# Kernel optimization log

Measured on AMD Instinct MI355X. Metric: run time of the kernel, lower is better.

## Reference

```python
import jax, jax.numpy as jnp
import numpy as np

# cfg.SIAMESE constants (typical FastVOD values)
ROIS_PER_IMAGE = 128
FG_PER_IMAGE = 32          # round(0.25 * 128)
FG_THRESH = 0.7
BG_THRESH_HI = 0.3
BG_THRESH_LO = 0.0

B, N, G = 16, 65536, 64


def _make_boxes(key, shape, img=1000.0):
    k1, k2, k3, k4 = jax.random.split(key, 4)
    x1 = jax.random.uniform(k1, shape) * (img - 64.0)
    y1 = jax.random.uniform(k2, shape) * (img - 64.0)
    w = jax.random.uniform(k3, shape) * 200.0 + 8.0
    h = jax.random.uniform(k4, shape) * 200.0 + 8.0
    return jnp.stack([x1, y1, jnp.minimum(x1 + w, img), jnp.minimum(y1 + h, img)], axis=-1)


def setup_inputs() -> dict:
    key = jax.random.key(0)
    kr, kg, kl, kt, kp, kf, kb, km = jax.random.split(key, 8)
    roi_boxes = _make_boxes(kr, (B, N))                      # [B,N,4]
    all_rois = jnp.concatenate([jnp.zeros((B, N, 1)), roi_boxes], axis=-1)  # [B,N,5]
    gtb = _make_boxes(kg, (B, G))                            # [B,G,4]
    labels = jax.random.randint(kl, (B, G), 1, 31).astype(jnp.float32)
    tids = jax.random.randint(kt, (B, G), 0, 1000).astype(jnp.float32)
    # pad last 8 gt per image with zero boxes (common padding pattern)
    pad = jnp.arange(G) >= G - 8
    gtb = jnp.where(pad[None, :, None], 0.0, gtb)
    labels = jnp.where(pad[None, :], 0.0, labels)
    gt_boxes = jnp.concatenate([gtb, labels[..., None], tids[..., None]], axis=-1)  # [B,G,6]
    u_perm = jax.random.uniform(kp, (B, N + G))
    u_fg = jax.random.uniform(kf, (B, ROIS_PER_IMAGE))
    u_bg = jax.random.uniform(kb, (B, ROIS_PER_IMAGE))
    return {"all_rois": all_rois, "gt_boxes": gt_boxes, "u_perm": u_perm,
            "u_fg": u_fg, "u_bg": u_bg}


def _bbox_overlaps_batch(rois, gt):
    # rois: [B,Nt,5] (idx,x1,y1,x2,y2), gt: [B,G,4]
    a = rois[:, :, 1:5]
    aw = a[:, :, 2] - a[:, :, 0] + 1.0
    ah = a[:, :, 3] - a[:, :, 1] + 1.0
    gw = gt[:, :, 2] - gt[:, :, 0] + 1.0
    gh = gt[:, :, 3] - gt[:, :, 1] + 1.0
    area_a = aw * ah                                  # [B,Nt]
    area_g = gw * gh                                  # [B,G]
    iw = jnp.clip(jnp.minimum(a[:, :, None, 2], gt[:, None, :, 2])
                  - jnp.maximum(a[:, :, None, 0], gt[:, None, :, 0]) + 1.0, 0.0)
    ih = jnp.clip(jnp.minimum(a[:, :, None, 3], gt[:, None, :, 3])
                  - jnp.maximum(a[:, :, None, 1], gt[:, None, :, 1]) + 1.0, 0.0)
    inter = iw * ih                                   # [B,Nt,G]
    ov = inter / (area_a[:, :, None] + area_g[:, None, :] - inter)
    gt_zero = (gw == 1.0) & (gh == 1.0)
    a_zero = (aw == 1.0) & (ah == 1.0)
    ov = jnp.where(gt_zero[:, None, :], 0.0, ov)
    ov = jnp.where(a_zero[:, :, None], -1.0, ov)
    return ov


def _sample_one(max_ov, up, uf, ub):
    # max_ov: [Nt]; replicates the per-image fg/bg sampling loop, vectorized.
    R = ROIS_PER_IMAGE
    fg_mask = max_ov >= FG_THRESH
    bg_mask = ((max_ov < BG_THRESH_HI) & (max_ov >= BG_THRESH_LO)) | (max_ov < 0)
    fg_num = fg_mask.sum()
    bg_num = bg_mask.sum()
    # randomly-ordered fg (resp. bg) indices come first after the argsort
    fg_order = jnp.argsort(jnp.where(fg_mask, up, 2.0))
    bg_order = jnp.argsort(jnp.where(bg_mask, up, 2.0))
    both = (fg_num > 0) & (bg_num > 0)
    only_fg = (fg_num > 0) & (bg_num == 0)
    fg_this = jnp.where(both, jnp.minimum(FG_PER_IMAGE, fg_num),
                        jnp.where(only_fg, R, 0))
    pos = jnp.arange(R)
    # fg: permutation (no replacement) when both present, else uniform w/ replacement
    fg_repl = jnp.clip((uf * fg_num).astype(jnp.int32), 0, jnp.maximum(fg_num - 1, 0))
    fg_pick = jnp.where(only_fg, fg_order[fg_repl], fg_order[pos])
    # bg: always uniform with replacement
    bg_repl = jnp.clip((ub * bg_num).astype(jnp.int32), 0, jnp.maximum(bg_num - 1, 0))
    bg_pick = bg_order[bg_repl]
    is_fg = pos < fg_this
    keep = jnp.where(is_fg, fg_pick, bg_pick)
    return keep, is_fg


def reference(all_rois, gt_boxes, u_perm, u_fg, u_bg):
    # append gt boxes as proposals: [B, N+G, 5]
    gt_append = jnp.concatenate(
        [jnp.zeros_like(gt_boxes[:, :, :1]), gt_boxes[:, :, :4]], axis=-1)
    rois_all = jnp.concatenate([all_rois, gt_append], axis=1)
    ov = _bbox_overlaps_batch(rois_all, gt_boxes[:, :, :4])      # [B,Nt,G]
    max_ov = jnp.max(ov, axis=2)
    gt_assign = jnp.argmax(ov, axis=2)                            # [B,Nt]
    labels = jnp.take_along_axis(gt_boxes[:, :, 4], gt_assign, axis=1)   # [B,Nt]
    tids = jnp.take_along_axis(gt_boxes[:, :, 5], gt_assign, axis=1)
    keep, is_fg = jax.vmap(_sample_one)(max_ov, u_perm, u_fg, u_bg)      # [B,R]
    lab_b = jnp.where(is_fg, jnp.take_along_axis(labels, keep, axis=1), 0.0)
    tid_b = jnp.where(is_fg, jnp.take_along_axis(tids, keep, axis=1), -1.0)
    rois_b = jnp.take_along_axis(rois_all, keep[:, :, None], axis=1)     # [B,R,5]
    batch_idx = jnp.arange(rois_b.shape[0], dtype=rois_b.dtype)[:, None]
    rois_b = rois_b.at[:, :, 0].set(jnp.broadcast_to(batch_idx, rois_b.shape[:2]))
    return rois_b, lab_b, tid_b
```

## Files before the change

kernel.cpp:

```cpp
#include <hip/hip_runtime.h>

#define B_   16
#define N_   65536
#define G_   64
#define M_   (N_ + G_)
#define R_   128
#define FGP  32
#define NB_  16384
#define NCH_ 32
#define CHUNK_ (NB_ / NCH_)
#define NROW_ 32
#define FW_  (NB_ / 32)
#define TPB_  256

__global__ void prep_kernel(const float* __restrict__ gt_boxes,
                            int*    __restrict__ zbase,
                            float4* __restrict__ gt4,
                            float*  __restrict__ garea,
                            int*    __restrict__ jmax)
{
    const int gid = blockIdx.x * blockDim.x + threadIdx.x;
    const int total = NROW_ * NB_ + NROW_ * FW_;
    for (int idx = gid; idx < total; idx += gridDim.x * blockDim.x) zbase[idx] = 0;
    if (gid < B_ * G_) {
        int b = gid >> 6, j = gid & 63;
        const float* g = gt_boxes + gid * 6;
        float x1 = g[0], y1 = g[1], x2 = g[2], y2 = g[3];
        float gw = x2 - x1 + 1.0f, gh = y2 - y1 + 1.0f;
        bool gz = (gw == 1.0f) && (gh == 1.0f);
        gt4[gid] = gz ? make_float4(3.0e8f, 3.0e8f, -3.0e8f, -3.0e8f)
                      : make_float4(x1, y1, x2, y2);
        garea[gid] = gw * gh;
        unsigned long long alive = __ballot(!gz);
        if (j == 0) { int last = 63 - __clzll(alive); jmax[b] = (last + 8) & ~7; }
    }
}

__global__ void iou_kernel(const float* __restrict__ all_rois,
                           const float* __restrict__ gt_boxes,
                           const float4* __restrict__ gt4,
                           const float*  __restrict__ garea,
                           const int*    __restrict__ jmax,
                           const float*  __restrict__ u_perm,
                           unsigned*     __restrict__ packed,
                           int*          __restrict__ hist)
{
    __shared__ float4 sg[G_];
    __shared__ float  sa[G_];
    const int b   = blockIdx.y;
    const int tid = threadIdx.x;
    if (tid < G_) { sg[tid] = gt4[b * G_ + tid]; sa[tid] = garea[b * G_ + tid]; }
    __syncthreads();

    const int i = blockIdx.x * blockDim.x + tid;
    if (i >= M_) return;

    float x1, y1, x2, y2;
    if (i < N_) {
        const float* p = all_rois + ((size_t)b * N_ + i) * 5;
        x1 = p[1]; y1 = p[2]; x2 = p[3]; y2 = p[4];
    } else {
        const float* p = gt_boxes + (b * G_ + (i - N_)) * 6;
        x1 = p[0]; y1 = p[1]; x2 = p[2]; y2 = p[3];
    }
    float aw = x2 - x1 + 1.0f, ah = y2 - y1 + 1.0f;
    float area_a = aw * ah;
    bool  a_zero = (aw == 1.0f) && (ah == 1.0f);

    const int jm = jmax[b];
    float ib = 0.0f, sb = 1.0f;
    for (int jj = 0; jj < jm; jj += 8) {
        #pragma unroll
        for (int kk = 0; kk < 8; ++kk) {
            const int j = jj + kk;
            const float4 g  = sg[j];
            const float  ga = sa[j];
            float iw  = fmaxf(fminf(x2, g.z) - fmaxf(x1, g.x) + 1.0f, 0.0f);
            float ih2 = fmaxf(fminf(y2, g.w) - fmaxf(y1, g.y) + 1.0f, 0.0f);
            float inter = iw * ih2;
            float s     = area_a + ga;
            float hi1 = inter * sb, lo1 = fmaf(inter, sb, -hi1);
            float hi2 = ib * s,     lo2 = fmaf(ib, s, -hi2);
            bool gt = (hi1 > hi2) || ((hi1 == hi2) && (lo1 > lo2));
            if (gt) { ib = inter; sb = s; }
        }
    }
    float best = ib / (sb - ib);
    if (a_zero) best = -1.0f;

    bool fg = best >= 0.7f;
    bool bg = best < 0.3f;
    unsigned pk = 0xFFFFFFFFu;
    if (fg || bg) {
        int cls = fg ? 0 : 1;
        float u = u_perm[(size_t)b * M_ + i];
        int bucket = min(max((int)(u * (float)NB_), 0), NB_ - 1);
        pk = ((unsigned)cls << 16) | (unsigned)bucket;
        atomicAdd(&hist[(size_t)(b * 2 + cls) * NB_ + bucket], 1);
    }
    packed[(size_t)b * M_ + i] = pk;
}

__global__ __launch_bounds__(512) void scanflag_kernel(
    int*      __restrict__ hist,
    unsigned* __restrict__ flags,
    const float* __restrict__ u_fg,
    const float* __restrict__ u_bg,
    int4*     __restrict__ pick)
{
    __shared__ int scoarse[2][NCH_];
    __shared__ int scnt[2];
    __shared__ int swt[2][8], swb[2][8];
    const int bb  = blockIdx.x;
    const int tid = threadIdx.x;
    const int lane = tid & 63, w = tid >> 6;

    for (int rr = 0; rr < 2; ++rr) {
        const int row = bb * 2 + rr;
        int4* h4 = (int4*)(hist + (size_t)row * NB_ + tid * 32);
        int v[32];
        #pragma unroll
        for (int q = 0; q < 8; ++q) {
            int4 x4 = h4[q];
            v[q*4] = x4.x; v[q*4+1] = x4.y; v[q*4+2] = x4.z; v[q*4+3] = x4.w;
        }
        int run = 0;
        #pragma unroll
        for (int q = 0; q < 32; ++q) { int x = v[q]; v[q] = run; run += x; }
        int x = run;
        #pragma unroll
        for (int d = 1; d < 64; d <<= 1) {
            int y = __shfl_up(x, d);
            if (lane >= d) x += y;
        }
        if (lane == 63) swt[rr][w] = x;
        __syncthreads();
        if (tid == 0) {
            int a = 0;
            #pragma unroll
            for (int q = 0; q < 8; ++q) { swb[rr][q] = a; a += swt[rr][q]; }
        }
        __syncthreads();
        const int incl  = swb[rr][w] + x;
        const int texcl = incl - run;
        #pragma unroll
        for (int q = 0; q < 8; ++q) {
            h4[q] = make_int4(v[q*4] + texcl, v[q*4+1] + texcl,
                              v[q*4+2] + texcl, v[q*4+3] + texcl);
        }
        if ((tid & 15) == 15) scoarse[rr][tid >> 4] = incl;
        if (tid == 511) scnt[rr] = incl;
    }
    __syncthreads();

    if (tid < R_) {
        const int pos = tid;
        const int fgn = scnt[0], bgn = scnt[1];
        const bool both    = (fgn > 0) && (bgn > 0);
        const bool only_fg = (fgn > 0) && (bgn == 0);
        const int fg_this  = both ? min(FGP, fgn) : (only_fg ? R_ : 0);
        const bool is_fg   = pos < fg_this;
        int cls, rank, cnum;
        if (is_fg) {
            cls = 0; cnum = fgn;
            if (only_fg) {
                float uf = u_fg[bb * R_ + pos];
                int kk = (int)(uf * (float)fgn);
                rank = min(max(kk, 0), max(fgn - 1, 0));
            } else {
                rank = pos;
            }
        } else {
            cls = 1; cnum = bgn;
            float ubv = u_bg[bb * R_ + pos];
            int kk = (int)(ubv * (float)bgn);
            rank = min(max(kk, 0), max(bgn - 1, 0));
        }
        int4 p4 = make_int4(0, 0, 0, is_fg ? 1 : 0);
        if (cnum > 0) {
            const int row = bb * 2 + cls;
            const int* sce = scoarse[cls];
            int c = 0;
            while (c < NCH_ - 1 && sce[c] <= rank) ++c;
            const int* Er = hist + (size_t)row * NB_;
            int lo = c * CHUNK_, hi = c * CHUNK_ + CHUNK_ - 1;
            while (lo < hi) {
                int mid = (lo + hi + 1) >> 1;
                if (Er[mid] <= rank) lo = mid; else hi = mid - 1;
            }
            const int start = Er[lo];
            const int next  = (lo < NB_ - 1) ? Er[lo + 1] : cnum;
            atomicOr(&flags[row * FW_ + (lo >> 5)], 1u << (lo & 31));
            p4 = make_int4(start, next - start, rank - start, is_fg ? 1 : 0);
        }
        pick[bb * R_ + pos] = p4;
    }
}

__global__ void scatter_kernel(const unsigned* __restrict__ packed,
                               const unsigned* __restrict__ flags,
                               int*            __restrict__ E,
                               int*            __restrict__ buckets)
{
    const int b  = blockIdx.y;
    const int i4 = blockIdx.x * blockDim.x + threadIdx.x;
    if (i4 >= M_ / 4) return;
    const uint4 p = ((const uint4*)(packed + (size_t)b * M_))[i4];
    const unsigned pks[4] = { p.x, p.y, p.z, p.w };
    #pragma unroll
    for (int k = 0; k < 4; ++k) {
        unsigned pk = pks[k];
        if (pk == 0xFFFFFFFFu) continue;
        const int cls = (int)(pk >> 16);
        const int bucket = (int)(pk & 0xFFFFu);
        const int row = b * 2 + cls;
        unsigned w = flags[row * FW_ + (bucket >> 5)];
        if (!(w & (1u << (bucket & 31)))) continue;
        int pp = atomicAdd(&E[(size_t)row * NB_ + bucket], 1);
        buckets[(size_t)row * M_ + pp] = i4 * 4 + k;
    }
}

__global__ void sample_kernel(const float* __restrict__ all_rois,
                              const float* __restrict__ gt_boxes,
                              const float4* __restrict__ gt4,
                              const float*  __restrict__ garea,
                              const float* __restrict__ u_perm,
                              const int4* __restrict__ pick,
                              const int*  __restrict__ buckets,
                              float*      __restrict__ out)
{
    const int b   = blockIdx.x;
    const int pos = threadIdx.x;
    const int4 pk = pick[b * R_ + pos];
    const bool is_fg = pk.w != 0;
    const int  cls   = is_fg ? 0 : 1;

    int keep = 0;
    if (pk.y > 0) {
        const int row = b * 2 + cls;
        const int*   be = buckets + (size_t)row * M_ + pk.x;
        const float* up = u_perm + (size_t)b * M_;
        const int cnt2 = pk.y, r = pk.z;
        for (int t2 = 0; t2 < cnt2; ++t2) {
            int it = be[t2]; float ut = up[it];
            int rk = 0;
            for (int s2 = 0; s2 < cnt2; ++s2) {
                if (s2 == t2) continue;
                int is2 = be[s2]; float us = up[is2];
                if (us < ut || (us == ut && is2 < it)) rk++;
            }
            if (rk == r) { keep = it; break; }
        }
    }

    float ox1, oy1, ox2, oy2;
    if (keep < N_) {
        const float* p = all_rois + ((size_t)b * N_ + keep) * 5;
        ox1 = p[1]; oy1 = p[2]; ox2 = p[3]; oy2 = p[4];
    } else {
        const float* p = gt_boxes + (b * G_ + (keep - N_)) * 6;
        ox1 = p[0]; oy1 = p[1]; ox2 = p[2]; oy2 = p[3];
    }
    float* ro = out + ((size_t)b * R_ + pos) * 5;
    ro[0] = (float)b; ro[1] = ox1; ro[2] = oy1; ro[3] = ox2; ro[4] = oy2;

    float lab = 0.0f, tidv = -1.0f;
    if (is_fg) {
        float aw = ox2 - ox1 + 1.0f, ah = oy2 - oy1 + 1.0f;
        float area_a = aw * ah;
        float bestv = -1e30f;
        int   bi    = 0;
        for (int j = 0; j < G_; ++j) {
            const float4 g  = gt4[b * G_ + j];
            const float  ga = garea[b * G_ + j];
            float iw  = fmaxf(fminf(ox2, g.z) - fmaxf(ox1, g.x) + 1.0f, 0.0f);
            float ih2 = fmaxf(fminf(oy2, g.w) - fmaxf(oy1, g.y) + 1.0f, 0.0f);
            float inter = iw * ih2;
            float ov = inter / (area_a + ga - inter);
            if (ov > bestv) { bestv = ov; bi = j; }
        }
        lab  = gt_boxes[(b * G_ + bi) * 6 + 4];
        tidv = gt_boxes[(b * G_ + bi) * 6 + 5];
    }
    out[(size_t)B_ * R_ * 5 + b * R_ + pos] = lab;
    out[(size_t)B_ * R_ * 5 + (size_t)B_ * R_ + b * R_ + pos] = tidv;
}

extern "C" void kernel_launch(void* const* d_in, const int* in_sizes, int n_in,
                              void* d_out, int out_size, void* d_ws, size_t ws_size,
                              hipStream_t stream)
{
    const float* all_rois = (const float*)d_in[0];
    const float* gt_boxes = (const float*)d_in[1];
    const float* u_perm   = (const float*)d_in[2];
    const float* u_fg     = (const float*)d_in[3];
    const float* u_bg     = (const float*)d_in[4];
    float* out = (float*)d_out;

    int*      hist    = (int*)d_ws;
    unsigned* flags   = (unsigned*)(hist + (size_t)NROW_ * NB_);
    int4*     pick    = (int4*)(flags + NROW_ * FW_);
    unsigned* packed  = (unsigned*)(pick + B_ * R_);
    int*      buckets = (int*)(packed + (size_t)B_ * M_);
    float4*   gt4     = (float4*)(buckets + (size_t)NROW_ * M_);
    float*    garea   = (float*)(gt4 + B_ * G_);
    int*      jmax    = (int*)(garea + B_ * G_);

    prep_kernel<<<512, TPB_, 0, stream>>>(gt_boxes, hist, gt4, garea, jmax);

    dim3 grid1((M_ + TPB_ - 1) / TPB_, B_);
    iou_kernel<<<grid1, TPB_, 0, stream>>>(all_rois, gt_boxes, gt4, garea, jmax,
                                           u_perm, packed, hist);
    scanflag_kernel<<<B_, 512, 0, stream>>>(hist, flags, u_fg, u_bg, pick);

    dim3 grid3((M_ / 4 + TPB_ - 1) / TPB_, B_);
    scatter_kernel<<<grid3, TPB_, 0, stream>>>(packed, flags, hist, buckets);
    sample_kernel<<<B_, R_, 0, stream>>>(all_rois, gt_boxes, gt4, garea,
                                         u_perm, pick, buckets, out);
}
```

Baseline: 101.8 us.

## Fuse scan, scatter and sample into one per-image tail kernel; two ROIs per thread

```diff
diff --git a/kernel.cpp b/kernel.cpp
--- a/kernel.cpp
+++ b/kernel.cpp
@@ -4,6 +4,7 @@
 #define N_   65536
 #define G_   64
 #define M_   (N_ + G_)
+#define HALF_ 32800
 #define R_   128
 #define FGP  32
 #define NB_  16384
@@ -14,14 +15,13 @@
 #define TPB_  256
 
 __global__ void prep_kernel(const float* __restrict__ gt_boxes,
-                            int*    __restrict__ zbase,
+                            int*    __restrict__ hist,
                             float4* __restrict__ gt4,
                             float*  __restrict__ garea,
                             int*    __restrict__ jmax)
 {
     const int gid = blockIdx.x * blockDim.x + threadIdx.x;
-    const int total = NROW_ * NB_ + NROW_ * FW_;
-    for (int idx = gid; idx < total; idx += gridDim.x * blockDim.x) zbase[idx] = 0;
+    for (int idx = gid; idx < NROW_ * NB_; idx += gridDim.x * blockDim.x) hist[idx] = 0;
     if (gid < B_ * G_) {
         int b = gid >> 6, j = gid & 63;
         const float* g = gt_boxes + gid * 6;
@@ -52,105 +52,147 @@
     if (tid < G_) { sg[tid] = gt4[b * G_ + tid]; sa[tid] = garea[b * G_ + tid]; }
     __syncthreads();
 
-    const int i = blockIdx.x * blockDim.x + tid;
-    if (i >= M_) return;
-
-    float x1, y1, x2, y2;
-    if (i < N_) {
-        const float* p = all_rois + ((size_t)b * N_ + i) * 5;
-        x1 = p[1]; y1 = p[2]; x2 = p[3]; y2 = p[4];
+    const int i0 = blockIdx.x * TPB_ + tid;
+    if (i0 >= HALF_) return;
+    const int i1 = i0 + HALF_;
+
+    float ax1, ay1, ax2, ay2, bx1, by1, bx2, by2;
+    {
+        const float* p = all_rois + ((size_t)b * N_ + i0) * 5;
+        ax1 = p[1]; ay1 = p[2]; ax2 = p[3]; ay2 = p[4];
+    }
+    if (i1 < N_) {
+        const float* p = all_rois + ((size_t)b * N_ + i1) * 5;
+        bx1 = p[1]; by1 = p[2]; bx2 = p[3]; by2 = p[4];
     } else {
-        const float* p = gt_boxes + (b * G_ + (i - N_)) * 6;
-        x1 = p[0]; y1 = p[1]; x2 = p[2]; y2 = p[3];
-    }
-    float aw = x2 - x1 + 1.0f, ah = y2 - y1 + 1.0f;
-    float area_a = aw * ah;
-    bool  a_zero = (aw == 1.0f) && (ah == 1.0f);
+        const float* p = gt_boxes + (b * G_ + (i1 - N_)) * 6;
+        bx1 = p[0]; by1 = p[1]; bx2 = p[2]; by2 = p[3];
+    }
+    float awA = ax2 - ax1 + 1.0f, ahA = ay2 - ay1 + 1.0f, areaA = awA * ahA;
+    bool  azA = (awA == 1.0f) && (ahA == 1.0f);
+    float awB = bx2 - bx1 + 1.0f, ahB = by2 - by1 + 1.0f, areaB = awB * ahB;
+    bool  azB = (awB == 1.0f) && (ahB == 1.0f);
 
     const int jm = jmax[b];
-    float ib = 0.0f, sb = 1.0f;
+    float ibA = 0.0f, sbA = 1.0f, ibB = 0.0f, sbB = 1.0f;
     for (int jj = 0; jj < jm; jj += 8) {
         #pragma unroll
         for (int kk = 0; kk < 8; ++kk) {
             const int j = jj + kk;
             const float4 g  = sg[j];
             const float  ga = sa[j];
-            float iw  = fmaxf(fminf(x2, g.z) - fmaxf(x1, g.x) + 1.0f, 0.0f);
-            float ih2 = fmaxf(fminf(y2, g.w) - fmaxf(y1, g.y) + 1.0f, 0.0f);
-            float inter = iw * ih2;
-            float s     = area_a + ga;
-            float hi1 = inter * sb, lo1 = fmaf(inter, sb, -hi1);
-            float hi2 = ib * s,     lo2 = fmaf(ib, s, -hi2);
-            bool gt = (hi1 > hi2) || ((hi1 == hi2) && (lo1 > lo2));
-            if (gt) { ib = inter; sb = s; }
-        }
-    }
-    float best = ib / (sb - ib);
-    if (a_zero) best = -1.0f;
-
-    bool fg = best >= 0.7f;
-    bool bg = best < 0.3f;
-    unsigned pk = 0xFFFFFFFFu;
-    if (fg || bg) {
-        int cls = fg ? 0 : 1;
-        float u = u_perm[(size_t)b * M_ + i];
-        int bucket = min(max((int)(u * (float)NB_), 0), NB_ - 1);
-        pk = ((unsigned)cls << 16) | (unsigned)bucket;
-        atomicAdd(&hist[(size_t)(b * 2 + cls) * NB_ + bucket], 1);
-    }
-    packed[(size_t)b * M_ + i] = pk;
+            float iwA = fmaxf(fminf(ax2, g.z) - fmaxf(ax1, g.x) + 1.0f, 0.0f);
+            float ihA = fmaxf(fminf(ay2, g.w) - fmaxf(ay1, g.y) + 1.0f, 0.0f);
+            float inA = iwA * ihA;
+            float sA  = areaA + ga;
+            float h1 = inA * sbA, l1 = fmaf(inA, sbA, -h1);
+            float h2 = ibA * sA,  l2 = fmaf(ibA, sA, -h2);
+            if ((h1 > h2) || ((h1 == h2) && (l1 > l2))) { ibA = inA; sbA = sA; }
+            float iwB = fmaxf(fminf(bx2, g.z) - fmaxf(bx1, g.x) + 1.0f, 0.0f);
+            float ihB = fmaxf(fminf(by2, g.w) - fmaxf(by1, g.y) + 1.0f, 0.0f);
+            float inB = iwB * ihB;
+            float sB  = areaB + ga;
+            float h3 = inB * sbB, l3 = fmaf(inB, sbB, -h3);
+            float h4 = ibB * sB,  l4 = fmaf(ibB, sB, -h4);
+            if ((h3 > h4) || ((h3 == h4) && (l3 > l4))) { ibB = inB; sbB = sB; }
+        }
+    }
+
+    {
+        float best = ibA / (sbA - ibA);
+        if (azA) best = -1.0f;
+        bool fg = best >= 0.7f, bg = best < 0.3f;
+        unsigned pk = 0xFFFFFFFFu;
+        if (fg || bg) {
+            int cls = fg ? 0 : 1;
+            float u = u_perm[(size_t)b * M_ + i0];
+            int bucket = min(max((int)(u * (float)NB_), 0), NB_ - 1);
+            pk = ((unsigned)cls << 16) | (unsigned)bucket;
+            atomicAdd(&hist[(size_t)(b * 2 + cls) * NB_ + bucket], 1);
+        }
+        packed[(size_t)b * M_ + i0] = pk;
+    }
+    {
+        float best = ibB / (sbB - ibB);
+        if (azB) best = -1.0f;
+        bool fg = best >= 0.7f, bg = best < 0.3f;
+        unsigned pk = 0xFFFFFFFFu;
+        if (fg || bg) {
+            int cls = fg ? 0 : 1;
+            float u = u_perm[(size_t)b * M_ + i1];
+            int bucket = min(max((int)(u * (float)NB_), 0), NB_ - 1);
+            pk = ((unsigned)cls << 16) | (unsigned)bucket;
+            atomicAdd(&hist[(size_t)(b * 2 + cls) * NB_ + bucket], 1);
+        }
+        packed[(size_t)b * M_ + i1] = pk;
+    }
 }
 
-__global__ __launch_bounds__(512) void scanflag_kernel(
-    int*      __restrict__ hist,
-    unsigned* __restrict__ flags,
+__global__ __launch_bounds__(1024) void tail_kernel(
+    const float* __restrict__ all_rois,
+    const float* __restrict__ gt_boxes,
+    const float4* __restrict__ gt4,
+    const float*  __restrict__ garea,
+    const float* __restrict__ u_perm,
     const float* __restrict__ u_fg,
     const float* __restrict__ u_bg,
-    int4*     __restrict__ pick)
+    const unsigned* __restrict__ packed,
+    int*      __restrict__ hist,
+    int*      __restrict__ buckets,
+    float*    __restrict__ out)
 {
-    __shared__ int scoarse[2][NCH_];
-    __shared__ int scnt[2];
-    __shared__ int swt[2][8], swb[2][8];
+    __shared__ float4   sg[G_];
+    __shared__ float    sa[G_];
+    __shared__ unsigned sflags[2 * FW_];
+    __shared__ int      scoarse[2][NCH_];
+    __shared__ int      scnt[2];
+    __shared__ int      swt[2][8], swb[2][8];
+    __shared__ int4     spick[R_];
+
     const int bb  = blockIdx.x;
     const int tid = threadIdx.x;
-    const int lane = tid & 63, w = tid >> 6;
-
-    for (int rr = 0; rr < 2; ++rr) {
-        const int row = bb * 2 + rr;
-        int4* h4 = (int4*)(hist + (size_t)row * NB_ + tid * 32);
-        int v[32];
+    const int rr  = tid >> 9;
+    const int t   = tid & 511;
+    const int lane = tid & 63, w = (tid >> 6) & 7;
+
+    sflags[tid] = 0;
+    if (tid < G_) { sg[tid] = gt4[bb * G_ + tid]; sa[tid] = garea[bb * G_ + tid]; }
+
+    const int row = bb * 2 + rr;
+    int4* h4 = (int4*)(hist + (size_t)row * NB_ + t * 32);
+    int v[32];
+    #pragma unroll
+    for (int q = 0; q < 8; ++q) {
+        int4 x4 = h4[q];
+        v[q*4] = x4.x; v[q*4+1] = x4.y; v[q*4+2] = x4.z; v[q*4+3] = x4.w;
+    }
+    int run = 0;
+    #pragma unroll
+    for (int q = 0; q < 32; ++q) { int x = v[q]; v[q] = run; run += x; }
+    int x = run;
+    #pragma unroll
+    for (int d = 1; d < 64; d <<= 1) {
+        int y = __shfl_up(x, d);
+        if (lane >= d) x += y;
+    }
+    if (lane == 63) swt[rr][w] = x;
+    __syncthreads();
+    if ((tid & 511) == 0) {
+        int a = 0;
         #pragma unroll
-        for (int q = 0; q < 8; ++q) {
-            int4 x4 = h4[q];
-            v[q*4] = x4.x; v[q*4+1] = x4.y; v[q*4+2] = x4.z; v[q*4+3] = x4.w;
-        }
-        int run = 0;
-        #pragma unroll
-        for (int q = 0; q < 32; ++q) { int x = v[q]; v[q] = run; run += x; }
-        int x = run;
-        #pragma unroll
-        for (int d = 1; d < 64; d <<= 1) {
-            int y = __shfl_up(x, d);
-            if (lane >= d) x += y;
-        }
-        if (lane == 63) swt[rr][w] = x;
-        __syncthreads();
-        if (tid == 0) {
-            int a = 0;
-            #pragma unroll
-            for (int q = 0; q < 8; ++q) { swb[rr][q] = a; a += swt[rr][q]; }
-        }
-        __syncthreads();
-        const int incl  = swb[rr][w] + x;
-        const int texcl = incl - run;
-        #pragma unroll
-        for (int q = 0; q < 8; ++q) {
-            h4[q] = make_int4(v[q*4] + texcl, v[q*4+1] + texcl,
-                              v[q*4+2] + texcl, v[q*4+3] + texcl);
-        }
-        if ((tid & 15) == 15) scoarse[rr][tid >> 4] = incl;
-        if (tid == 511) scnt[rr] = incl;
-    }
+        for (int q = 0; q < 8; ++q) { swb[rr][q] = a; a += swt[rr][q]; }
+        scnt[rr] = a;
+    }
+    __syncthreads();
+    const int incl  = swb[rr][w] + x;
+    const int texcl = incl - run;
+    #pragma unroll
+    for (int q = 0; q < 8; ++q) {
+        h4[q] = make_int4(v[q*4] + texcl, v[q*4+1] + texcl,
+                          v[q*4+2] + texcl, v[q*4+3] + texcl);
+    }
+    if ((t & 15) == 15) scoarse[rr][t >> 4] = incl;
+    __threadfence();
     __syncthreads();
 
     if (tid < R_) {
@@ -178,11 +220,10 @@
         }
         int4 p4 = make_int4(0, 0, 0, is_fg ? 1 : 0);
         if (cnum > 0) {
-            const int row = bb * 2 + cls;
             const int* sce = scoarse[cls];
             int c = 0;
             while (c < NCH_ - 1 && sce[c] <= rank) ++c;
-            const int* Er = hist + (size_t)row * NB_;
+            const int* Er = hist + (size_t)(bb * 2 + cls) * NB_;
             int lo = c * CHUNK_, hi = c * CHUNK_ + CHUNK_ - 1;
             while (lo < hi) {
                 int mid = (lo + hi + 1) >> 1;
@@ -190,101 +231,89 @@
             }
             const int start = Er[lo];
             const int next  = (lo < NB_ - 1) ? Er[lo + 1] : cnum;
-            atomicOr(&flags[row * FW_ + (lo >> 5)], 1u << (lo & 31));
+            atomicOr(&sflags[cls * FW_ + (lo >> 5)], 1u << (lo & 31));
             p4 = make_int4(start, next - start, rank - start, is_fg ? 1 : 0);
         }
-        pick[bb * R_ + pos] = p4;
-    }
-}
-
-__global__ void scatter_kernel(const unsigned* __restrict__ packed,
-                               const unsigned* __restrict__ flags,
-                               int*            __restrict__ E,
-                               int*            __restrict__ buckets)
-{
-    const int b  = blockIdx.y;
-    const int i4 = blockIdx.x * blockDim.x + threadIdx.x;
-    if (i4 >= M_ / 4) return;
-    const uint4 p = ((const uint4*)(packed + (size_t)b * M_))[i4];
-    const unsigned pks[4] = { p.x, p.y, p.z, p.w };
-    #pragma unroll
-    for (int k = 0; k < 4; ++k) {
-        unsigned pk = pks[k];
-        if (pk == 0xFFFFFFFFu) continue;
-        const int cls = (int)(pk >> 16);
-        const int bucket = (int)(pk & 0xFFFFu);
-        const int row = b * 2 + cls;
-        unsigned w = flags[row * FW_ + (bucket >> 5)];
-        if (!(w & (1u << (bucket & 31)))) continue;
-        int pp = atomicAdd(&E[(size_t)row * NB_ + bucket], 1);
-        buckets[(size_t)row * M_ + pp] = i4 * 4 + k;
-    }
-}
-
-__global__ void sample_kernel(const float* __restrict__ all_rois,
-                              const float* __restrict__ gt_boxes,
-                              const float4* __restrict__ gt4,
-                              const float*  __restrict__ garea,
-                              const float* __restrict__ u_perm,
-                              const int4* __restrict__ pick,
-                              const int*  __restrict__ buckets,
-                              float*      __restrict__ out)
-{
-    const int b   = blockIdx.x;
-    const int pos = threadIdx.x;
-    const int4 pk = pick[b * R_ + pos];
-    const bool is_fg = pk.w != 0;
-    const int  cls   = is_fg ? 0 : 1;
-
-    int keep = 0;
-    if (pk.y > 0) {
-        const int row = b * 2 + cls;
-        const int*   be = buckets + (size_t)row * M_ + pk.x;
-        const float* up = u_perm + (size_t)b * M_;
-        const int cnt2 = pk.y, r = pk.z;
-        for (int t2 = 0; t2 < cnt2; ++t2) {
-            int it = be[t2]; float ut = up[it];
-            int rk = 0;
-            for (int s2 = 0; s2 < cnt2; ++s2) {
-                if (s2 == t2) continue;
-                int is2 = be[s2]; float us = up[is2];
-                if (us < ut || (us == ut && is2 < it)) rk++;
-            }
-            if (rk == r) { keep = it; break; }
-        }
-    }
-
-    float ox1, oy1, ox2, oy2;
-    if (keep < N_) {
-        const float* p = all_rois + ((size_t)b * N_ + keep) * 5;
-        ox1 = p[1]; oy1 = p[2]; ox2 = p[3]; oy2 = p[4];
-    } else {
-        const float* p = gt_boxes + (b * G_ + (keep - N_)) * 6;
-        ox1 = p[0]; oy1 = p[1]; ox2 = p[2]; oy2 = p[3];
-    }
-    float* ro = out + ((size_t)b * R_ + pos) * 5;
-    ro[0] = (float)b; ro[1] = ox1; ro[2] = oy1; ro[3] = ox2; ro[4] = oy2;
-
-    float lab = 0.0f, tidv = -1.0f;
-    if (is_fg) {
-        float aw = ox2 - ox1 + 1.0f, ah = oy2 - oy1 + 1.0f;
-        float area_a = aw * ah;
-        float bestv = -1e30f;
-        int   bi    = 0;
-        for (int j = 0; j < G_; ++j) {
-            const float4 g  = gt4[b * G_ + j];
-            const float  ga = garea[b * G_ + j];
-            float iw  = fmaxf(fminf(ox2, g.z) - fmaxf(ox1, g.x) + 1.0f, 0.0f);
-            float ih2 = fmaxf(fminf(oy2, g.w) - fmaxf(oy1, g.y) + 1.0f, 0.0f);
-            float inter = iw * ih2;
-            float ov = inter / (area_a + ga - inter);
-            if (ov > bestv) { bestv = ov; bi = j; }
-        }
-        lab  = gt_boxes[(b * G_ + bi) * 6 + 4];
-        tidv = gt_boxes[(b * G_ + bi) * 6 + 5];
-    }
-    out[(size_t)B_ * R_ * 5 + b * R_ + pos] = lab;
-    out[(size_t)B_ * R_ * 5 + (size_t)B_ * R_ + b * R_ + pos] = tidv;
+        spick[pos] = p4;
+    }
+    __syncthreads();
+
+    {
+        const uint4* pb = (const uint4*)(packed + (size_t)bb * M_);
+        for (int it2 = 0; it2 < 17; ++it2) {
+            const int i4 = it2 * 1024 + tid;
+            if (i4 >= M_ / 4) break;
+            const uint4 pv = pb[i4];
+            const unsigned arr[4] = { pv.x, pv.y, pv.z, pv.w };
+            #pragma unroll
+            for (int k = 0; k < 4; ++k) {
+                unsigned pk = arr[k];
+                if (pk == 0xFFFFFFFFu) continue;
+                const int cls = (int)(pk >> 16);
+                const int bucket = (int)(pk & 0xFFFFu);
+                unsigned wd = sflags[cls * FW_ + (bucket >> 5)];
+                if (!(wd & (1u << (bucket & 31)))) continue;
+                int pp = atomicAdd(&hist[(size_t)(bb * 2 + cls) * NB_ + bucket], 1);
+                buckets[(size_t)(bb * 2 + cls) * M_ + pp] = i4 * 4 + k;
+            }
+        }
+    }
+    __threadfence();
+    __syncthreads();
+
+    if (tid < R_) {
+        const int pos = tid;
+        const int4 p4 = spick[pos];
+        const bool is_fg = p4.w != 0;
+        const int  cls   = is_fg ? 0 : 1;
+        int keep = 0;
+        if (p4.y > 0) {
+            const int*   be = buckets + (size_t)(bb * 2 + cls) * M_ + p4.x;
+            const float* up = u_perm + (size_t)bb * M_;
+            const int cnt2 = p4.y, r = p4.z;
+            for (int t2 = 0; t2 < cnt2; ++t2) {
+                int it2 = be[t2]; float ut = up[it2];
+                int rk = 0;
+                for (int s2 = 0; s2 < cnt2; ++s2) {
+                    if (s2 == t2) continue;
+                    int is2 = be[s2]; float us = up[is2];
+                    if (us < ut || (us == ut && is2 < it2)) rk++;
+                }
+                if (rk == r) { keep = it2; break; }
+            }
+        }
+        float ox1, oy1, ox2, oy2;
+        if (keep < N_) {
+            const float* p = all_rois + ((size_t)bb * N_ + keep) * 5;
+            ox1 = p[1]; oy1 = p[2]; ox2 = p[3]; oy2 = p[4];
+        } else {
+            const float* p = gt_boxes + (bb * G_ + (keep - N_)) * 6;
+            ox1 = p[0]; oy1 = p[1]; ox2 = p[2]; oy2 = p[3];
+        }
+        float* ro = out + ((size_t)bb * R_ + pos) * 5;
+        ro[0] = (float)bb; ro[1] = ox1; ro[2] = oy1; ro[3] = ox2; ro[4] = oy2;
+
+        float lab = 0.0f, tidv = -1.0f;
+        if (is_fg) {
+            float aw = ox2 - ox1 + 1.0f, ah = oy2 - oy1 + 1.0f;
+            float area_a = aw * ah;
+            float bestv = -1e30f;
+            int   bi    = 0;
+            for (int j = 0; j < G_; ++j) {
+                const float4 g  = sg[j];
+                const float  ga = sa[j];
+                float iw  = fmaxf(fminf(ox2, g.z) - fmaxf(ox1, g.x) + 1.0f, 0.0f);
+                float ih2 = fmaxf(fminf(oy2, g.w) - fmaxf(oy1, g.y) + 1.0f, 0.0f);
+                float inter = iw * ih2;
+                float ov = inter / (area_a + ga - inter);
+                if (ov > bestv) { bestv = ov; bi = j; }
+            }
+            lab  = gt_boxes[(bb * G_ + bi) * 6 + 4];
+            tidv = gt_boxes[(bb * G_ + bi) * 6 + 5];
+        }
+        out[(size_t)B_ * R_ * 5 + bb * R_ + pos] = lab;
+        out[(size_t)B_ * R_ * 5 + (size_t)B_ * R_ + bb * R_ + pos] = tidv;
+    }
 }
 
 extern "C" void kernel_launch(void* const* d_in, const int* in_sizes, int n_in,
@@ -299,9 +328,7 @@
     float* out = (float*)d_out;
 
     int*      hist    = (int*)d_ws;
-    unsigned* flags   = (unsigned*)(hist + (size_t)NROW_ * NB_);
-    int4*     pick    = (int4*)(flags + NROW_ * FW_);
-    unsigned* packed  = (unsigned*)(pick + B_ * R_);
+    unsigned* packed  = (unsigned*)(hist + (size_t)NROW_ * NB_);
     int*      buckets = (int*)(packed + (size_t)B_ * M_);
     float4*   gt4     = (float4*)(buckets + (size_t)NROW_ * M_);
     float*    garea   = (float*)(gt4 + B_ * G_);
@@ -309,13 +336,10 @@
 
     prep_kernel<<<512, TPB_, 0, stream>>>(gt_boxes, hist, gt4, garea, jmax);
 
-    dim3 grid1((M_ + TPB_ - 1) / TPB_, B_);
+    dim3 grid1((HALF_ + TPB_ - 1) / TPB_, B_);
     iou_kernel<<<grid1, TPB_, 0, stream>>>(all_rois, gt_boxes, gt4, garea, jmax,
                                            u_perm, packed, hist);
-    scanflag_kernel<<<B_, 512, 0, stream>>>(hist, flags, u_fg, u_bg, pick);
-
-    dim3 grid3((M_ / 4 + TPB_ - 1) / TPB_, B_);
-    scatter_kernel<<<grid3, TPB_, 0, stream>>>(packed, flags, hist, buckets);
-    sample_kernel<<<B_, R_, 0, stream>>>(all_rois, gt_boxes, gt4, garea,
-                                         u_perm, pick, buckets, out);
+    tail_kernel<<<B_, 1024, 0, stream>>>(all_rois, gt_boxes, gt4, garea,
+                                         u_perm, u_fg, u_bg, packed,
+                                         hist, buckets, out);
 }
```

New measurement: 126.3 us. 1.24x slower.

## Drop prep kernel, build GT tile in-block, 4 ROIs per thread in IoU

Applied to the files above, without the earlier changes.

```diff
diff --git a/kernel.cpp b/kernel.cpp
--- a/kernel.cpp
+++ b/kernel.cpp
@@ -4,6 +4,7 @@
 #define N_   65536
 #define G_   64
 #define M_   (N_ + G_)
+#define Q_   16400
 #define R_   128
 #define FGP  32
 #define NB_  16384
@@ -13,92 +14,97 @@
 #define FW_  (NB_ / 32)
 #define TPB_  256
 
-__global__ void prep_kernel(const float* __restrict__ gt_boxes,
-                            int*    __restrict__ zbase,
-                            float4* __restrict__ gt4,
-                            float*  __restrict__ garea,
-                            int*    __restrict__ jmax)
-{
-    const int gid = blockIdx.x * blockDim.x + threadIdx.x;
-    const int total = NROW_ * NB_ + NROW_ * FW_;
-    for (int idx = gid; idx < total; idx += gridDim.x * blockDim.x) zbase[idx] = 0;
-    if (gid < B_ * G_) {
-        int b = gid >> 6, j = gid & 63;
-        const float* g = gt_boxes + gid * 6;
+__device__ __forceinline__ void build_gt_tile(const float* __restrict__ gt_boxes,
+                                              int b, int tid,
+                                              float4* sg, float* sa, int* sjm)
+{
+    if (tid < G_) {
+        const float* g = gt_boxes + (b * G_ + tid) * 6;
         float x1 = g[0], y1 = g[1], x2 = g[2], y2 = g[3];
         float gw = x2 - x1 + 1.0f, gh = y2 - y1 + 1.0f;
         bool gz = (gw == 1.0f) && (gh == 1.0f);
-        gt4[gid] = gz ? make_float4(3.0e8f, 3.0e8f, -3.0e8f, -3.0e8f)
-                      : make_float4(x1, y1, x2, y2);
-        garea[gid] = gw * gh;
+        sg[tid] = gz ? make_float4(3.0e8f, 3.0e8f, -3.0e8f, -3.0e8f)
+                     : make_float4(x1, y1, x2, y2);
+        sa[tid] = gw * gh;
         unsigned long long alive = __ballot(!gz);
-        if (j == 0) { int last = 63 - __clzll(alive); jmax[b] = (last + 8) & ~7; }
-    }
-}
-
-__global__ void iou_kernel(const float* __restrict__ all_rois,
-                           const float* __restrict__ gt_boxes,
-                           const float4* __restrict__ gt4,
-                           const float*  __restrict__ garea,
-                           const int*    __restrict__ jmax,
-                           const float*  __restrict__ u_perm,
-                           unsigned*     __restrict__ packed,
-                           int*          __restrict__ hist)
+        if (tid == 0) { int last = 63 - __clzll(alive); *sjm = (last + 8) & ~7; }
+    }
+    __syncthreads();
+}
+
+__global__ __launch_bounds__(TPB_, 4) void iou_kernel(
+    const float* __restrict__ all_rois,
+    const float* __restrict__ gt_boxes,
+    const float* __restrict__ u_perm,
+    unsigned*    __restrict__ packed,
+    int*         __restrict__ hist)
 {
     __shared__ float4 sg[G_];
     __shared__ float  sa[G_];
+    __shared__ int    sjm;
     const int b   = blockIdx.y;
     const int tid = threadIdx.x;
-    if (tid < G_) { sg[tid] = gt4[b * G_ + tid]; sa[tid] = garea[b * G_ + tid]; }
-    __syncthreads();
-
-    const int i = blockIdx.x * blockDim.x + tid;
-    if (i >= M_) return;
-
-    float x1, y1, x2, y2;
-    if (i < N_) {
-        const float* p = all_rois + ((size_t)b * N_ + i) * 5;
-        x1 = p[1]; y1 = p[2]; x2 = p[3]; y2 = p[4];
-    } else {
-        const float* p = gt_boxes + (b * G_ + (i - N_)) * 6;
-        x1 = p[0]; y1 = p[1]; x2 = p[2]; y2 = p[3];
-    }
-    float aw = x2 - x1 + 1.0f, ah = y2 - y1 + 1.0f;
-    float area_a = aw * ah;
-    bool  a_zero = (aw == 1.0f) && (ah == 1.0f);
-
-    const int jm = jmax[b];
-    float ib = 0.0f, sb = 1.0f;
-    for (int jj = 0; jj < jm; jj += 8) {
-        #pragma unroll
-        for (int kk = 0; kk < 8; ++kk) {
+    build_gt_tile(gt_boxes, b, tid, sg, sa, &sjm);
+
+    const int i0 = blockIdx.x * TPB_ + tid;
+    if (i0 >= Q_) return;
+    const int jm = sjm;
+
+    float X1[4], Y1[4], X2[4], Y2[4], AREA[4], IB[4], SB[4];
+    bool  AZ[4];
+    #pragma unroll
+    for (int r = 0; r < 4; ++r) {
+        const int i = i0 + r * Q_;
+        float x1, y1, x2, y2;
+        if (i < N_) {
+            const float* p = all_rois + ((size_t)b * N_ + i) * 5;
+            x1 = p[1]; y1 = p[2]; x2 = p[3]; y2 = p[4];
+        } else {
+            const float* p = gt_boxes + (b * G_ + (i - N_)) * 6;
+            x1 = p[0]; y1 = p[1]; x2 = p[2]; y2 = p[3];
+        }
+        float aw = x2 - x1 + 1.0f, ah = y2 - y1 + 1.0f;
+        X1[r] = x1; Y1[r] = y1; X2[r] = x2; Y2[r] = y2;
+        AREA[r] = aw * ah;
+        AZ[r] = (aw == 1.0f) && (ah == 1.0f);
+        IB[r] = 0.0f; SB[r] = 1.0f;
+    }
+
+    for (int jj = 0; jj < jm; jj += 4) {
+        #pragma unroll
+        for (int kk = 0; kk < 4; ++kk) {
             const int j = jj + kk;
             const float4 g  = sg[j];
             const float  ga = sa[j];
-            float iw  = fmaxf(fminf(x2, g.z) - fmaxf(x1, g.x) + 1.0f, 0.0f);
-            float ih2 = fmaxf(fminf(y2, g.w) - fmaxf(y1, g.y) + 1.0f, 0.0f);
-            float inter = iw * ih2;
-            float s     = area_a + ga;
-            float hi1 = inter * sb, lo1 = fmaf(inter, sb, -hi1);
-            float hi2 = ib * s,     lo2 = fmaf(ib, s, -hi2);
-            bool gt = (hi1 > hi2) || ((hi1 == hi2) && (lo1 > lo2));
-            if (gt) { ib = inter; sb = s; }
-        }
-    }
-    float best = ib / (sb - ib);
-    if (a_zero) best = -1.0f;
-
-    bool fg = best >= 0.7f;
-    bool bg = best < 0.3f;
-    unsigned pk = 0xFFFFFFFFu;
-    if (fg || bg) {
-        int cls = fg ? 0 : 1;
-        float u = u_perm[(size_t)b * M_ + i];
-        int bucket = min(max((int)(u * (float)NB_), 0), NB_ - 1);
-        pk = ((unsigned)cls << 16) | (unsigned)bucket;
-        atomicAdd(&hist[(size_t)(b * 2 + cls) * NB_ + bucket], 1);
-    }
-    packed[(size_t)b * M_ + i] = pk;
+            #pragma unroll
+            for (int r = 0; r < 4; ++r) {
+                float iw = fmaxf(fminf(X2[r], g.z) - fmaxf(X1[r], g.x) + 1.0f, 0.0f);
+                float ih = fmaxf(fminf(Y2[r], g.w) - fmaxf(Y1[r], g.y) + 1.0f, 0.0f);
+                float inter = iw * ih;
+                float s     = AREA[r] + ga;
+                float h1 = inter * SB[r], l1 = fmaf(inter, SB[r], -h1);
+                float h2 = IB[r] * s,     l2 = fmaf(IB[r], s, -h2);
+                if ((h1 > h2) || ((h1 == h2) && (l1 > l2))) { IB[r] = inter; SB[r] = s; }
+            }
+        }
+    }
+
+    #pragma unroll
+    for (int r = 0; r < 4; ++r) {
+        const int i = i0 + r * Q_;
+        float best = IB[r] / (SB[r] - IB[r]);
+        if (AZ[r]) best = -1.0f;
+        bool fg = best >= 0.7f, bg = best < 0.3f;
+        unsigned pk = 0xFFFFFFFFu;
+        if (fg || bg) {
+            int cls = fg ? 0 : 1;
+            float u = u_perm[(size_t)b * M_ + i];
+            int bucket = min(max((int)(u * (float)NB_), 0), NB_ - 1);
+            pk = ((unsigned)cls << 16) | (unsigned)bucket;
+            atomicAdd(&hist[(size_t)(b * 2 + cls) * NB_ + bucket], 1);
+        }
+        packed[(size_t)b * M_ + i] = pk;
+    }
 }
 
 __global__ __launch_bounds__(512) void scanflag_kernel(
@@ -108,12 +114,15 @@
     const float* __restrict__ u_bg,
     int4*     __restrict__ pick)
 {
+    __shared__ unsigned sflags[2 * FW_];
     __shared__ int scoarse[2][NCH_];
     __shared__ int scnt[2];
     __shared__ int swt[2][8], swb[2][8];
     const int bb  = blockIdx.x;
     const int tid = threadIdx.x;
     const int lane = tid & 63, w = tid >> 6;
+
+    sflags[tid] = 0; sflags[tid + 512] = 0;
 
     for (int rr = 0; rr < 2; ++rr) {
         const int row = bb * 2 + rr;
@@ -178,11 +187,10 @@
         }
         int4 p4 = make_int4(0, 0, 0, is_fg ? 1 : 0);
         if (cnum > 0) {
-            const int row = bb * 2 + cls;
             const int* sce = scoarse[cls];
             int c = 0;
             while (c < NCH_ - 1 && sce[c] <= rank) ++c;
-            const int* Er = hist + (size_t)row * NB_;
+            const int* Er = hist + (size_t)(bb * 2 + cls) * NB_;
             int lo = c * CHUNK_, hi = c * CHUNK_ + CHUNK_ - 1;
             while (lo < hi) {
                 int mid = (lo + hi + 1) >> 1;
@@ -190,11 +198,14 @@
             }
             const int start = Er[lo];
             const int next  = (lo < NB_ - 1) ? Er[lo + 1] : cnum;
-            atomicOr(&flags[row * FW_ + (lo >> 5)], 1u << (lo & 31));
+            atomicOr(&sflags[cls * FW_ + (lo >> 5)], 1u << (lo & 31));
             p4 = make_int4(start, next - start, rank - start, is_fg ? 1 : 0);
         }
         pick[bb * R_ + pos] = p4;
     }
+    __syncthreads();
+    flags[bb * 2 * FW_ + tid]       = sflags[tid];
+    flags[bb * 2 * FW_ + tid + 512] = sflags[tid + 512];
 }
 
 __global__ void scatter_kernel(const unsigned* __restrict__ packed,
@@ -223,23 +234,25 @@
 
 __global__ void sample_kernel(const float* __restrict__ all_rois,
                               const float* __restrict__ gt_boxes,
-                              const float4* __restrict__ gt4,
-                              const float*  __restrict__ garea,
                               const float* __restrict__ u_perm,
                               const int4* __restrict__ pick,
                               const int*  __restrict__ buckets,
                               float*      __restrict__ out)
 {
+    __shared__ float4 sg[G_];
+    __shared__ float  sa[G_];
+    __shared__ int    sjm;
     const int b   = blockIdx.x;
     const int pos = threadIdx.x;
+    build_gt_tile(gt_boxes, b, pos, sg, sa, &sjm);
+
     const int4 pk = pick[b * R_ + pos];
     const bool is_fg = pk.w != 0;
     const int  cls   = is_fg ? 0 : 1;
 
     int keep = 0;
     if (pk.y > 0) {
-        const int row = b * 2 + cls;
-        const int*   be = buckets + (size_t)row * M_ + pk.x;
+        const int*   be = buckets + (size_t)(b * 2 + cls) * M_ + pk.x;
         const float* up = u_perm + (size_t)b * M_;
         const int cnt2 = pk.y, r = pk.z;
         for (int t2 = 0; t2 < cnt2; ++t2) {
@@ -272,8 +285,8 @@
         float bestv = -1e30f;
         int   bi    = 0;
         for (int j = 0; j < G_; ++j) {
-            const float4 g  = gt4[b * G_ + j];
-            const float  ga = garea[b * G_ + j];
+            const float4 g  = sg[j];
+            const float  ga = sa[j];
             float iw  = fmaxf(fminf(ox2, g.z) - fmaxf(ox1, g.x) + 1.0f, 0.0f);
             float ih2 = fmaxf(fminf(oy2, g.w) - fmaxf(oy1, g.y) + 1.0f, 0.0f);
             float inter = iw * ih2;
@@ -303,19 +316,14 @@
     int4*     pick    = (int4*)(flags + NROW_ * FW_);
     unsigned* packed  = (unsigned*)(pick + B_ * R_);
     int*      buckets = (int*)(packed + (size_t)B_ * M_);
-    float4*   gt4     = (float4*)(buckets + (size_t)NROW_ * M_);
-    float*    garea   = (float*)(gt4 + B_ * G_);
-    int*      jmax    = (int*)(garea + B_ * G_);
-
-    prep_kernel<<<512, TPB_, 0, stream>>>(gt_boxes, hist, gt4, garea, jmax);
-
-    dim3 grid1((M_ + TPB_ - 1) / TPB_, B_);
-    iou_kernel<<<grid1, TPB_, 0, stream>>>(all_rois, gt_boxes, gt4, garea, jmax,
-                                           u_perm, packed, hist);
+
+    hipMemsetAsync(hist, 0, (size_t)NROW_ * NB_ * sizeof(int), stream);
+
+    dim3 grid1((Q_ + TPB_ - 1) / TPB_, B_);
+    iou_kernel<<<grid1, TPB_, 0, stream>>>(all_rois, gt_boxes, u_perm, packed, hist);
     scanflag_kernel<<<B_, 512, 0, stream>>>(hist, flags, u_fg, u_bg, pick);
 
     dim3 grid3((M_ / 4 + TPB_ - 1) / TPB_, B_);
     scatter_kernel<<<grid3, TPB_, 0, stream>>>(packed, flags, hist, buckets);
-    sample_kernel<<<B_, R_, 0, stream>>>(all_rois, gt_boxes, gt4, garea,
-                                         u_perm, pick, buckets, out);
-}
+    sample_kernel<<<B_, R_, 0, stream>>>(all_rois, gt_boxes, u_perm, pick, buckets, out);
+}
```

After: 111.5 us. +9.6%, slower.
